# Performance work log

Hardware: AMD Instinct MI355X
Metric: run time of the kernel (lower is better)

## Reference

```python
import jax, jax.numpy as jnp
import numpy as np

F = 26            # number of categorical fields
V_FIELD = 8000    # vocab per field
V = F * V_FIELD   # 208000, size of every shared-index table
D_EMB = 16
DNN_IN = F * F * D_EMB  # 10816
H1, H2 = 256, 128
BS = 4096
NUM_DENSE = 13
EPS = 1e-5


def setup_inputs() -> dict:
    key = jax.random.key(0)
    ks = jax.random.split(key, 16)
    def n(k, shape, s=0.05):
        return jax.random.normal(k, shape, dtype=jnp.float32) * s
    return {
        "X_sparse": jax.random.randint(ks[0], (BS, F), 0, V_FIELD, dtype=jnp.int32),
        "X_dense": jax.random.normal(ks[1], (BS, NUM_DENSE), dtype=jnp.float32),
        "fm1_emb": n(ks[2], (V, 1)),
        "bias": jnp.zeros((1,), jnp.float32),
        "fm1_dense_W": n(ks[3], (1, NUM_DENSE)),
        "fm1_dense_b": jnp.zeros((1,), jnp.float32),
        "emb_tables": n(ks[4], (F, V, D_EMB)),  # one table per field (FFM)
        "dense_W": n(ks[5], (DNN_IN, NUM_DENSE)),
        "dense_b": jnp.zeros((DNN_IN,), jnp.float32),
        "W1": n(ks[6], (H1, DNN_IN)),
        "b1": jnp.zeros((H1,), jnp.float32),
        "g1": jnp.ones((H1,), jnp.float32),
        "beta1": jnp.zeros((H1,), jnp.float32),
        "W2": n(ks[7], (H2, H1)),
        "b2": jnp.zeros((H2,), jnp.float32),
        "g2": jnp.ones((H2,), jnp.float32),
        "beta2": jnp.zeros((H2,), jnp.float32),
        "Wout": n(ks[8], (1, H2)),
        "bout": jnp.zeros((1,), jnp.float32),
    }


def _bn(x, g, b):
    # BatchNorm1d in training mode: biased batch statistics
    m = jnp.mean(x, axis=0)
    v = jnp.var(x, axis=0)
    return (x - m) * jax.lax.rsqrt(v + EPS) * g + b


def reference(X_sparse, X_dense, fm1_emb, bias, fm1_dense_W, fm1_dense_b,
              emb_tables, dense_W, dense_b,
              W1, b1, g1, beta1, W2, b2, g2, beta2, Wout, bout):
    offsets = (jnp.arange(F, dtype=X_sparse.dtype) * V_FIELD)[None, :]
    X = X_sparse + offsets                      # [bs, F] global indices

    # FM first order
    fm1 = jnp.sum(fm1_emb[X], axis=1) + bias    # [bs, 1]
    fm1 = fm1 + X_dense @ fm1_dense_W.T + fm1_dense_b

    # FFM second order: E[t, b, f, d] = table t looked up at field f's index
    E = emb_tables[:, X, :]                     # [F, bs, F, d]
    A = jnp.transpose(E, (1, 0, 2, 3))          # [bs, F_table, F_field, d]
    # pair (i<j): xs[j][:, i] * xs[i][:, j] = A[b, i, j] * A[b, j, i]
    P = A * jnp.swapaxes(A, 1, 2)               # [bs, F, F, d]
    mask = jnp.triu(jnp.ones((F, F), jnp.float32), 1)
    fm2 = jnp.einsum('bijd,ij->b', P, mask)[:, None]  # [bs, 1]

    # DNN: concat per-table lookups then flatten -> [bs, F*F*d]
    dnn = A.reshape(A.shape[0], DNN_IN)
    dnn = dnn + jax.nn.relu(X_dense @ dense_W.T + dense_b)
    h = jax.nn.relu(_bn(dnn @ W1.T + b1, g1, beta1))  # dropout is identity (eval)
    h = jax.nn.relu(_bn(h @ W2.T + b2, g2, beta2))
    out = h @ Wout.T + bout
    return jax.nn.sigmoid(fm1 + fm2 + out)
```

## Files before the change

### kernel.cpp

```cpp
#include <hip/hip_runtime.h>

typedef __bf16 bf16x8 __attribute__((ext_vector_type(8)));
typedef float f32x4 __attribute__((ext_vector_type(4)));

#define F_FIELDS 26
#define V_FIELD  8000
#define V_TOT    208000
#define D_EMBD   16
#define DNN_IN   10816
#define BS       4096
#define ND       13
#define H1_DIM   256
#define H2_DIM   128
#define NP1      8

__device__ __forceinline__ unsigned short f2bf(float f) {
  unsigned u = __float_as_uint(f);
  u += 0x7fffu + ((u >> 16) & 1u);
  return (unsigned short)(u >> 16);
}
__device__ __forceinline__ float bf2f(unsigned short h) {
  return __uint_as_float(((unsigned)h) << 16);
}
__device__ __forceinline__ float bflo(unsigned u) { return __uint_as_float(u << 16); }
__device__ __forceinline__ float bfhi(unsigned u) { return __uint_as_float(u & 0xffff0000u); }
__device__ __forceinline__ unsigned packbf(float a, float b) {
  return (unsigned)f2bf(a) | ((unsigned)f2bf(b) << 16);
}

__device__ __forceinline__ void gload16(const void* g, void* l) {
  __builtin_amdgcn_global_load_lds(
      (const __attribute__((address_space(1))) unsigned int*)g,
      (__attribute__((address_space(3))) unsigned int*)l, 16, 0, 0);
}

__device__ __forceinline__ float dot8bf(uint4 a, uint4 b) {
  const unsigned* pa = (const unsigned*)&a;
  const unsigned* pb = (const unsigned*)&b;
  float s = 0.f;
#pragma unroll
  for (int k = 0; k < 4; ++k)
    s += bflo(pa[k]) * bflo(pb[k]) + bfhi(pa[k]) * bfhi(pb[k]);
  return s;
}

__global__ __launch_bounds__(256) void k_gather(
    const int* __restrict__ Xs, const float* __restrict__ emb,
    const float* __restrict__ fm1_emb, const float* __restrict__ bias,
    const float* __restrict__ fm1dW, const float* __restrict__ fm1db,
    const float* __restrict__ Xd,
    const float* __restrict__ W1, const float* __restrict__ W2,
    unsigned short* __restrict__ W1b, unsigned short* __restrict__ W2b,
    unsigned short* __restrict__ Abf, float* __restrict__ fm12) {
  const int b = blockIdx.x;
  const int tid = threadIdx.x;
  const int lane = tid & 63, wave = tid >> 6;
  __shared__ int   sidx[F_FIELDS];
  __shared__ float sc1[F_FIELDS];
  __shared__ __align__(16) unsigned short As[676 * 16];
  __shared__ float wred[4];

  if (tid < F_FIELDS) {
    int v = Xs[b * F_FIELDS + tid] + tid * V_FIELD;
    sidx[tid] = v;
    sc1[tid] = fm1_emb[v];
  }
  __syncthreads();

  const int q = tid & 3, rbase = tid >> 2;
  float4 vv[11];
#pragma unroll
  for (int it = 0; it < 11; ++it) {
    int r = rbase + it * 64;
    if (r < 676) {
      int i = r / 26, j = r - i * 26;
      const float* src = emb + ((size_t)i * V_TOT + sidx[j]) * D_EMBD + q * 4;
      vv[it] = *(const float4*)src;
    }
  }
  const int n1 = H1_DIM * DNN_IN, n2 = H2_DIM * H1_DIM;
  for (int t = b * 256 + tid; t < n1 + n2; t += BS * 256) {
    if (t < n1) W1b[t] = f2bf(W1[t]);
    else        W2b[t - n1] = f2bf(W2[t - n1]);
  }
#pragma unroll
  for (int it = 0; it < 11; ++it) {
    int r = rbase + it * 64;
    if (r < 676) {
      ushort4 u;
      u.x = f2bf(vv[it].x); u.y = f2bf(vv[it].y);
      u.z = f2bf(vv[it].z); u.w = f2bf(vv[it].w);
      *(ushort4*)&As[r * 16 + q * 4] = u;
      *(ushort4*)&Abf[(size_t)b * DNN_IN + r * 16 + q * 4] = u;
    }
  }
  __syncthreads();

  float acc2 = 0.f;
  for (int p = tid; p < 325; p += 256) {
    float disc = sqrtf((float)(2601 - 8 * p));
    int i = (int)((51.f - disc) * 0.5f);
    int cum = 25 * i - ((i * (i - 1)) >> 1);
    int j = i + 1 + (p - cum);
    const unsigned short* r1 = &As[(i * 26 + j) * 16];
    const unsigned short* r2 = &As[(j * 26 + i) * 16];
    acc2 += dot8bf(*(const uint4*)r1, *(const uint4*)r2);
    acc2 += dot8bf(*(const uint4*)(r1 + 8), *(const uint4*)(r2 + 8));
  }
#pragma unroll
  for (int off = 32; off; off >>= 1) acc2 += __shfl_down(acc2, off);
  if (lane == 0) wred[wave] = acc2;
  __syncthreads();
  if (tid == 0) {
    float fm2 = wred[0] + wred[1] + wred[2] + wred[3];
    float f1 = bias[0] + fm1db[0];
#pragma unroll
    for (int j = 0; j < F_FIELDS; ++j) f1 += sc1[j];
    for (int k = 0; k < ND; ++k) f1 += Xd[b * ND + k] * fm1dW[k];
    fm12[b] = f1 + fm2;
  }
}

__global__ __launch_bounds__(256) void k_dense(
    const float* __restrict__ Xd, const float* __restrict__ dW,
    const float* __restrict__ db_, unsigned short* __restrict__ Dnn) {
  const int t = threadIdx.x;
  const int eg = blockIdx.x * 256 + t;
  const int y0 = blockIdx.y * 64;
  __shared__ float sXd[64 * 13];
  for (int i = t; i < 64 * 13; i += 256) sXd[i] = Xd[y0 * 13 + i];
  __syncthreads();
  if (eg >= DNN_IN / 4) return;
  const int e = eg * 4;
  float wrg[4][13], brg[4];
#pragma unroll
  for (int j = 0; j < 4; ++j) {
    brg[j] = db_[e + j];
#pragma unroll
    for (int k = 0; k < 13; ++k) wrg[j][k] = dW[(e + j) * 13 + k];
  }
  uint2* dp = (uint2*)Dnn;
  for (int s0 = 0; s0 < 64; s0 += 8) {
    uint2 v[8];
#pragma unroll
    for (int u = 0; u < 8; ++u)
      v[u] = dp[(size_t)(y0 + s0 + u) * (DNN_IN / 4) + eg];
#pragma unroll
    for (int u = 0; u < 8; ++u) {
      const float* xr = &sXd[(s0 + u) * 13];
      float d0 = brg[0], d1 = brg[1], d2 = brg[2], d3 = brg[3];
#pragma unroll
      for (int k = 0; k < 13; ++k) {
        float xk = xr[k];
        d0 += wrg[0][k] * xk; d1 += wrg[1][k] * xk;
        d2 += wrg[2][k] * xk; d3 += wrg[3][k] * xk;
      }
      float a0 = bflo(v[u].x) + fmaxf(d0, 0.f);
      float a1 = bfhi(v[u].x) + fmaxf(d1, 0.f);
      float a2 = bflo(v[u].y) + fmaxf(d2, 0.f);
      float a3 = bfhi(v[u].y) + fmaxf(d3, 0.f);
      uint2 o; o.x = packbf(a0, a1); o.y = packbf(a2, a3);
      dp[(size_t)(y0 + s0 + u) * (DNN_IN / 4) + eg] = o;
    }
  }
}

__global__ __launch_bounds__(256) void k_gemm1(
    const unsigned short* __restrict__ A, const unsigned short* __restrict__ B,
    float* __restrict__ C) {
  __shared__ __align__(16) unsigned short sA[3][64 * 32];
  __shared__ __align__(16) unsigned short sB[3][256 * 32];
  const int tid = threadIdx.x;
  const int lane = tid & 63, w = tid >> 6;
  const int id = blockIdx.x;
  const int p = id & 7, mt = id >> 3;
  const int m0 = mt * 64;
  const int s0 = (338 * p) >> 3, s1 = (338 * (p + 1)) >> 3;
  C += (size_t)p * ((size_t)BS * H1_DIM);

  const int q = tid & 3, rr = tid >> 2;
  const unsigned short* gA  = A + (size_t)(m0 + rr) * DNN_IN + q * 8;
  const unsigned short* gB0 = B + (size_t)rr * DNN_IN + q * 8;
  const int fr = lane & 15, fk = lane >> 4;
  const int oA = fr * 32 + fk * 8;
  const int oB = (w * 64 + fr) * 32 + fk * 8;

  f32x4 acc[4][4] = {};

#define STAGE1(ks, bi) do { const int ko_ = (ks) * 32;                      \
    gload16(gA + ko_, &sA[bi][tid * 8]);                                    \
    gload16(gB0 + ko_, &sB[bi][tid * 8]);                                   \
    gload16(gB0 + (size_t)64 * DNN_IN + ko_, &sB[bi][2048 + tid * 8]);      \
    gload16(gB0 + (size_t)128 * DNN_IN + ko_, &sB[bi][4096 + tid * 8]);     \
    gload16(gB0 + (size_t)192 * DNN_IN + ko_, &sB[bi][6144 + tid * 8]); } while (0)

  STAGE1(s0, 0);
  if (s0 + 1 < s1) STAGE1(s0 + 1, 1);
  if (s0 + 2 < s1) STAGE1(s0 + 2, 2);

  int bi = 0;
  for (int ks = s0; ks < s1; ++ks) {
    if (ks + 2 < s1)      asm volatile("s_waitcnt vmcnt(10)" ::: "memory");
    else if (ks + 1 < s1) asm volatile("s_waitcnt vmcnt(5)" ::: "memory");
    else                  asm volatile("s_waitcnt vmcnt(0)" ::: "memory");
    __builtin_amdgcn_sched_barrier(0);
    __builtin_amdgcn_s_barrier();
    bf16x8 av[4], bv[4];
#pragma unroll
    for (int mi = 0; mi < 4; ++mi) av[mi] = *(const bf16x8*)&sA[bi][oA + mi * 512];
#pragma unroll
    for (int ni = 0; ni < 4; ++ni) bv[ni] = *(const bf16x8*)&sB[bi][oB + ni * 512];
    asm volatile("s_waitcnt lgkmcnt(0)" ::: "memory");
    __builtin_amdgcn_sched_barrier(0);
    __builtin_amdgcn_s_barrier();
    if (ks + 3 < s1) STAGE1(ks + 3, bi);
#pragma unroll
    for (int mi = 0; mi < 4; ++mi)
#pragma unroll
      for (int ni = 0; ni < 4; ++ni)
        acc[mi][ni] = __builtin_amdgcn_mfma_f32_16x16x32_bf16(
            av[mi], bv[ni], acc[mi][ni], 0, 0, 0);
    bi = bi + 1; if (bi == 3) bi = 0;
  }
#pragma unroll
  for (int mi = 0; mi < 4; ++mi)
#pragma unroll
    for (int ni = 0; ni < 4; ++ni)
#pragma unroll
      for (int r = 0; r < 4; ++r) {
        int row = m0 + mi * 16 + fk * 4 + r;
        int col = w * 64 + ni * 16 + fr;
        C[(size_t)row * H1_DIM + col] = acc[mi][ni][r];
      }
#undef STAGE1
}

__global__ __launch_bounds__(256) void k_stat1(
    const float* __restrict__ Yp, const float* __restrict__ b1,
    float* __restrict__ Y1, float* __restrict__ ps, float* __restrict__ pq) {
  const int g = blockIdx.x, n = threadIdx.x;
  const size_t plane = (size_t)BS * H1_DIM;
  float s = 0.f, s2 = 0.f;
  float bn = b1[n];
  for (int bb = 0; bb < 16; ++bb) {
    size_t o = (size_t)(g * 16 + bb) * H1_DIM + n;
    float y = bn;
#pragma unroll
    for (int pp = 0; pp < NP1; ++pp) y += Yp[o + pp * plane];
    Y1[o] = y; s += y; s2 += y * y;
  }
  ps[g * H1_DIM + n] = s;
  pq[g * H1_DIM + n] = s2;
}

__global__ __launch_bounds__(256) void k_apply1(
    const float* __restrict__ Y1, const float* __restrict__ ps,
    const float* __restrict__ pq, const float* __restrict__ g1,
    const float* __restrict__ be1, unsigned short* __restrict__ H1b) {
  const int g = blockIdx.x, n = threadIdx.x;
  float s = 0.f, s2 = 0.f;
  for (int gg = 0; gg < 256; ++gg) {
    s += ps[gg * H1_DIM + n];
    s2 += pq[gg * H1_DIM + n];
  }
  float m = s * (1.f / BS);
  float v = s2 * (1.f / BS) - m * m;
  float r = rsqrtf(v + 1e-5f);
  float ga = g1[n], bb_ = be1[n];
  for (int bb = 0; bb < 16; ++bb) {
    size_t o = (size_t)(g * 16 + bb) * H1_DIM + n;
    float h = (Y1[o] - m) * r * ga + bb_;
    H1b[o] = f2bf(fmaxf(h, 0.f));
  }
}

__global__ __launch_bounds__(256) void k_gemm2(
    const unsigned short* __restrict__ A, const unsigned short* __restrict__ B,
    const float* __restrict__ b2, float* __restrict__ Y2,
    float* __restrict__ ps, float* __restrict__ pq) {
  __shared__ __align__(16) unsigned short sA[2][128 * 32];
  __shared__ __align__(16) unsigned short sB[2][128 * 32];
  __shared__ float redS[8][H2_DIM];
  __shared__ float redQ[8][H2_DIM];
  const int tid = threadIdx.x;
  const int lane = tid & 63, wave = tid >> 6;
  const int m0 = blockIdx.x * 128;

  const int q = tid & 3, rr = tid >> 2;
  const unsigned short* gA0 = A + (size_t)(m0 + rr) * H1_DIM + q * 8;
  const unsigned short* gA1 = gA0 + (size_t)64 * H1_DIM;
  const unsigned short* gB0 = B + (size_t)rr * H1_DIM + q * 8;
  const unsigned short* gB1 = gB0 + (size_t)64 * H1_DIM;
  const int lo = wave * 512;

  const int wr = wave >> 1, wc = wave & 1;
  const int fr = lane & 15, fk = lane >> 4;
  const int oA = (wr * 64 + fr) * 32 + fk * 8;
  const int oB = (wc * 64 + fr) * 32 + fk * 8;

  f32x4 acc[4][4] = {};
  {
    gload16(gA0, &sA[0][lo]);
    gload16(gA1, &sA[0][2048 + lo]);
    gload16(gB0, &sB[0][lo]);
    gload16(gB1, &sB[0][2048 + lo]);
  }
  for (int ks = 0; ks < 8; ++ks) {
    const int cur = ks & 1;
    if (ks + 1 < 8) {
      const int ko = (ks + 1) * 32;
      gload16(gA0 + ko, &sA[cur ^ 1][lo]);
      gload16(gA1 + ko, &sA[cur ^ 1][2048 + lo]);
      gload16(gB0 + ko, &sB[cur ^ 1][lo]);
      gload16(gB1 + ko, &sB[cur ^ 1][2048 + lo]);
      asm volatile("s_waitcnt vmcnt(4)" ::: "memory");
    } else {
      asm volatile("s_waitcnt vmcnt(0)" ::: "memory");
    }
    __builtin_amdgcn_sched_barrier(0);
    __builtin_amdgcn_s_barrier();
    bf16x8 av[4], bv[4];
#pragma unroll
    for (int mi = 0; mi < 4; ++mi) av[mi] = *(const bf16x8*)&sA[cur][oA + mi * 512];
#pragma unroll
    for (int ni = 0; ni < 4; ++ni) bv[ni] = *(const bf16x8*)&sB[cur][oB + ni * 512];
    asm volatile("s_waitcnt lgkmcnt(0)" ::: "memory");
    __builtin_amdgcn_sched_barrier(0);
    __builtin_amdgcn_s_barrier();
#pragma unroll
    for (int mi = 0; mi < 4; ++mi)
#pragma unroll
      for (int ni = 0; ni < 4; ++ni)
        acc[mi][ni] = __builtin_amdgcn_mfma_f32_16x16x32_bf16(
            av[mi], bv[ni], acc[mi][ni], 0, 0, 0);
  }
  float sc[4] = {0.f, 0.f, 0.f, 0.f}, sq[4] = {0.f, 0.f, 0.f, 0.f};
#pragma unroll
  for (int ni = 0; ni < 4; ++ni) {
    int col = wc * 64 + ni * 16 + fr;
    float bcol = b2[col];
#pragma unroll
    for (int mi = 0; mi < 4; ++mi)
#pragma unroll
      for (int r = 0; r < 4; ++r) {
        int row = m0 + wr * 64 + mi * 16 + fk * 4 + r;
        float y = acc[mi][ni][r] + bcol;
        Y2[(size_t)row * H2_DIM + col] = y;
        sc[ni] += y; sq[ni] += y * y;
      }
  }
  const int slot = wr * 4 + fk;
#pragma unroll
  for (int ni = 0; ni < 4; ++ni) {
    int col = wc * 64 + ni * 16 + fr;
    redS[slot][col] = sc[ni];
    redQ[slot][col] = sq[ni];
  }
  __syncthreads();
  if (tid < H2_DIM) {
    float s = 0.f, s2 = 0.f;
#pragma unroll
    for (int sl = 0; sl < 8; ++sl) { s += redS[sl][tid]; s2 += redQ[sl][tid]; }
    ps[blockIdx.x * H2_DIM + tid] = s;
    pq[blockIdx.x * H2_DIM + tid] = s2;
  }
}

__global__ __launch_bounds__(256) void k_final(
    const float* __restrict__ Y2, const float* __restrict__ ps,
    const float* __restrict__ pq, const float* __restrict__ g2,
    const float* __restrict__ be2, const float* __restrict__ Wout,
    const float* __restrict__ bout, const float* __restrict__ fm12,
    float* __restrict__ out) {
  const int tid = threadIdx.x, wave = tid >> 6, lane = tid & 63;
  __shared__ float sm[H2_DIM], sr[H2_DIM], sg[H2_DIM], sbe[H2_DIM], sw[H2_DIM];
  if (tid < H2_DIM) {
    float s = 0.f, s2 = 0.f;
    for (int g = 0; g < 32; ++g) {
      s += ps[g * H2_DIM + tid];
      s2 += pq[g * H2_DIM + tid];
    }
    float m = s * (1.f / BS);
    float v = s2 * (1.f / BS) - m * m;
    sm[tid] = m; sr[tid] = rsqrtf(v + 1e-5f);
    sg[tid] = g2[tid]; sbe[tid] = be2[tid]; sw[tid] = Wout[tid];
  }
  __syncthreads();
  const float bo = bout[0];
  for (int ii = 0; ii < 16; ++ii) {
    int s = blockIdx.x * 64 + wave * 16 + ii;
    float acc = 0.f;
#pragma unroll
    for (int nn = 0; nn < 2; ++nn) {
      int n = lane + nn * 64;
      float y = Y2[(size_t)s * H2_DIM + n];
      float h = (y - sm[n]) * sr[n] * sg[n] + sbe[n];
      acc += fmaxf(h, 0.f) * sw[n];
    }
#pragma unroll
    for (int off = 32; off; off >>= 1) acc += __shfl_down(acc, off);
    if (lane == 0) {
      float logit = fm12[s] + acc + bo;
      out[s] = 1.f / (1.f + expf(-logit));
    }
  }
}

extern "C" void kernel_launch(void* const* d_in, const int* in_sizes, int n_in,
                              void* d_out, int out_size, void* d_ws, size_t ws_size,
                              hipStream_t stream) {
  const int*   Xs     = (const int*)d_in[0];
  const float* Xd     = (const float*)d_in[1];
  const float* fm1e   = (const float*)d_in[2];
  const float* bias   = (const float*)d_in[3];
  const float* fm1dW  = (const float*)d_in[4];
  const float* fm1db  = (const float*)d_in[5];
  const float* emb    = (const float*)d_in[6];
  const float* dW     = (const float*)d_in[7];
  const float* db_    = (const float*)d_in[8];
  const float* W1     = (const float*)d_in[9];
  const float* b1     = (const float*)d_in[10];
  const float* g1     = (const float*)d_in[11];
  const float* be1    = (const float*)d_in[12];
  const float* W2     = (const float*)d_in[13];
  const float* b2     = (const float*)d_in[14];
  const float* g2     = (const float*)d_in[15];
  const float* be2    = (const float*)d_in[16];
  const float* Wout   = (const float*)d_in[17];
  const float* bout   = (const float*)d_in[18];
  float* out = (float*)d_out;

  char* w = (char*)d_ws;
  unsigned short* Dnn = (unsigned short*)w; w += (size_t)BS * DNN_IN * 2;
  unsigned short* W1b = (unsigned short*)w; w += (size_t)H1_DIM * DNN_IN * 2;
  unsigned short* W2b = (unsigned short*)w; w += (size_t)H2_DIM * H1_DIM * 2;
  float* fm12 = (float*)w;  w += (size_t)BS * 4;
  float* Ypart = (float*)w; w += (size_t)NP1 * BS * H1_DIM * 4;
  float* Y1 = (float*)w;    w += (size_t)BS * H1_DIM * 4;
  unsigned short* H1b = (unsigned short*)w; w += (size_t)BS * H1_DIM * 2;
  float* Y2 = (float*)w;    w += (size_t)BS * H2_DIM * 4;
  float* ps1 = (float*)w;   w += 256 * H1_DIM * 4;
  float* pq1 = (float*)w;   w += 256 * H1_DIM * 4;
  float* ps2 = (float*)w;   w += 32 * H2_DIM * 4;
  float* pq2 = (float*)w;   w += 32 * H2_DIM * 4;

  k_gather<<<BS, 256, 0, stream>>>(Xs, emb, fm1e, bias, fm1dW, fm1db, Xd,
                                   W1, W2, W1b, W2b, Dnn, fm12);
  k_dense<<<dim3(11, 64), 256, 0, stream>>>(Xd, dW, db_, Dnn);
  k_gemm1<<<64 * NP1, 256, 0, stream>>>(Dnn, W1b, Ypart);
  k_stat1<<<256, 256, 0, stream>>>(Ypart, b1, Y1, ps1, pq1);
  k_apply1<<<256, 256, 0, stream>>>(Y1, ps1, pq1, g1, be1, H1b);
  k_gemm2<<<32, 256, 0, stream>>>(H1b, W2b, b2, Y2, ps2, pq2);
  k_final<<<BS / 64, 256, 0, stream>>>(Y2, ps2, pq2, g2, be2, Wout, bout, fm12, out);
}
```

Measured before the change: 213.0 us.

## Fuse dense-feature projection into GEMM1 via per-tile MFMA recompute

Removes the separate k_dense kernel, which read and rewrote the whole bf16 activation matrix. GEMM1 now computes relu(Xd·dW^T+db) on the fly for each K-tile with small MFMAs, using Xd padded with a bias column of ones and a bf16 dW laid out K-major. It then accumulates that tile against W1 as a second MFMA pass. This saves a full read-modify-write pass over the large activation buffer, at the cost of extra MFMAs, an extra LDS round trip and barrier per K step, and extra global loads in the pipeline.

```diff
diff --git a/kernel.cpp b/kernel.cpp
--- a/kernel.cpp
+++ b/kernel.cpp
@@ -24,9 +24,6 @@
 }
 __device__ __forceinline__ float bflo(unsigned u) { return __uint_as_float(u << 16); }
 __device__ __forceinline__ float bfhi(unsigned u) { return __uint_as_float(u & 0xffff0000u); }
-__device__ __forceinline__ unsigned packbf(float a, float b) {
-  return (unsigned)f2bf(a) | ((unsigned)f2bf(b) << 16);
-}
 
 __device__ __forceinline__ void gload16(const void* g, void* l) {
   __builtin_amdgcn_global_load_lds(
@@ -50,7 +47,9 @@
     const float* __restrict__ fm1dW, const float* __restrict__ fm1db,
     const float* __restrict__ Xd,
     const float* __restrict__ W1, const float* __restrict__ W2,
+    const float* __restrict__ dW, const float* __restrict__ db_,
     unsigned short* __restrict__ W1b, unsigned short* __restrict__ W2b,
+    unsigned short* __restrict__ dWb,
     unsigned short* __restrict__ Abf, float* __restrict__ fm12) {
   const int b = blockIdx.x;
   const int tid = threadIdx.x;
@@ -82,6 +81,16 @@
   for (int t = b * 256 + tid; t < n1 + n2; t += BS * 256) {
     if (t < n1) W1b[t] = f2bf(W1[t]);
     else        W2b[t - n1] = f2bf(W2[t - n1]);
+  }
+  for (int e = b * 256 + tid; e < DNN_IN; e += BS * 256) {
+    unsigned short row[32];
+#pragma unroll
+    for (int k = 0; k < 13; ++k) row[k] = f2bf(dW[e * 13 + k]);
+    row[13] = f2bf(db_[e]);
+#pragma unroll
+    for (int k = 14; k < 32; ++k) row[k] = 0;
+#pragma unroll
+    for (int k = 0; k < 32; ++k) dWb[e * 32 + k] = row[k];
   }
 #pragma unroll
   for (int it = 0; it < 11; ++it) {
@@ -121,55 +130,15 @@
   }
 }
 
-__global__ __launch_bounds__(256) void k_dense(
-    const float* __restrict__ Xd, const float* __restrict__ dW,
-    const float* __restrict__ db_, unsigned short* __restrict__ Dnn) {
-  const int t = threadIdx.x;
-  const int eg = blockIdx.x * 256 + t;
-  const int y0 = blockIdx.y * 64;
-  __shared__ float sXd[64 * 13];
-  for (int i = t; i < 64 * 13; i += 256) sXd[i] = Xd[y0 * 13 + i];
-  __syncthreads();
-  if (eg >= DNN_IN / 4) return;
-  const int e = eg * 4;
-  float wrg[4][13], brg[4];
-#pragma unroll
-  for (int j = 0; j < 4; ++j) {
-    brg[j] = db_[e + j];
-#pragma unroll
-    for (int k = 0; k < 13; ++k) wrg[j][k] = dW[(e + j) * 13 + k];
-  }
-  uint2* dp = (uint2*)Dnn;
-  for (int s0 = 0; s0 < 64; s0 += 8) {
-    uint2 v[8];
-#pragma unroll
-    for (int u = 0; u < 8; ++u)
-      v[u] = dp[(size_t)(y0 + s0 + u) * (DNN_IN / 4) + eg];
-#pragma unroll
-    for (int u = 0; u < 8; ++u) {
-      const float* xr = &sXd[(s0 + u) * 13];
-      float d0 = brg[0], d1 = brg[1], d2 = brg[2], d3 = brg[3];
-#pragma unroll
-      for (int k = 0; k < 13; ++k) {
-        float xk = xr[k];
-        d0 += wrg[0][k] * xk; d1 += wrg[1][k] * xk;
-        d2 += wrg[2][k] * xk; d3 += wrg[3][k] * xk;
-      }
-      float a0 = bflo(v[u].x) + fmaxf(d0, 0.f);
-      float a1 = bfhi(v[u].x) + fmaxf(d1, 0.f);
-      float a2 = bflo(v[u].y) + fmaxf(d2, 0.f);
-      float a3 = bfhi(v[u].y) + fmaxf(d3, 0.f);
-      uint2 o; o.x = packbf(a0, a1); o.y = packbf(a2, a3);
-      dp[(size_t)(y0 + s0 + u) * (DNN_IN / 4) + eg] = o;
-    }
-  }
-}
-
 __global__ __launch_bounds__(256) void k_gemm1(
     const unsigned short* __restrict__ A, const unsigned short* __restrict__ B,
+    const unsigned short* __restrict__ dWb, const float* __restrict__ Xd,
     float* __restrict__ C) {
   __shared__ __align__(16) unsigned short sA[3][64 * 32];
   __shared__ __align__(16) unsigned short sB[3][256 * 32];
+  __shared__ __align__(16) unsigned short sWd[3][1024];
+  __shared__ __align__(16) unsigned short sD[64 * 32];
+  __shared__ __align__(16) unsigned short sXd[64 * 32];
   const int tid = threadIdx.x;
   const int lane = tid & 63, w = tid >> 6;
   const int id = blockIdx.x;
@@ -178,6 +147,19 @@
   const int s0 = (338 * p) >> 3, s1 = (338 * (p + 1)) >> 3;
   C += (size_t)p * ((size_t)BS * H1_DIM);
 
+  if (tid < 64) {
+    const float* xr = Xd + (size_t)(m0 + tid) * ND;
+    unsigned short row[32];
+#pragma unroll
+    for (int k = 0; k < 13; ++k) row[k] = f2bf(xr[k]);
+    row[13] = 0x3F80;
+#pragma unroll
+    for (int k = 14; k < 32; ++k) row[k] = 0;
+#pragma unroll
+    for (int k = 0; k < 32; ++k) sXd[tid * 32 + k] = row[k];
+  }
+  __syncthreads();
+
   const int q = tid & 3, rr = tid >> 2;
   const unsigned short* gA  = A + (size_t)(m0 + rr) * DNN_IN + q * 8;
   const unsigned short* gB0 = B + (size_t)rr * DNN_IN + q * 8;
@@ -185,14 +167,23 @@
   const int oA = fr * 32 + fk * 8;
   const int oB = (w * 64 + fr) * 32 + fk * 8;
 
+  const bf16x8 avd = *(const bf16x8*)&sXd[(w * 16 + fr) * 32 + fk * 8];
+  const int oW0 = fr * 32 + fk * 8;
+  const int oW1 = (16 + fr) * 32 + fk * 8;
+  const int drow = w * 16 + fk * 4;
+
   f32x4 acc[4][4] = {};
+  const f32x4 zf = {0.f, 0.f, 0.f, 0.f};
 
 #define STAGE1(ks, bi) do { const int ko_ = (ks) * 32;                      \
     gload16(gA + ko_, &sA[bi][tid * 8]);                                    \
     gload16(gB0 + ko_, &sB[bi][tid * 8]);                                   \
     gload16(gB0 + (size_t)64 * DNN_IN + ko_, &sB[bi][2048 + tid * 8]);      \
     gload16(gB0 + (size_t)128 * DNN_IN + ko_, &sB[bi][4096 + tid * 8]);     \
-    gload16(gB0 + (size_t)192 * DNN_IN + ko_, &sB[bi][6144 + tid * 8]); } while (0)
+    gload16(gB0 + (size_t)192 * DNN_IN + ko_, &sB[bi][6144 + tid * 8]);     \
+    gload16(dWb + (size_t)ko_ * 32 + (size_t)lane * 8, &sWd[bi][lane * 8]); \
+    gload16(dWb + (size_t)ko_ * 32 + 512 + (size_t)lane * 8,                \
+            &sWd[bi][512 + lane * 8]); } while (0)
 
   STAGE1(s0, 0);
   if (s0 + 1 < s1) STAGE1(s0 + 1, 1);
@@ -200,11 +191,13 @@
 
   int bi = 0;
   for (int ks = s0; ks < s1; ++ks) {
-    if (ks + 2 < s1)      asm volatile("s_waitcnt vmcnt(10)" ::: "memory");
-    else if (ks + 1 < s1) asm volatile("s_waitcnt vmcnt(5)" ::: "memory");
+    if (ks + 2 < s1)      asm volatile("s_waitcnt vmcnt(14)" ::: "memory");
+    else if (ks + 1 < s1) asm volatile("s_waitcnt vmcnt(7)" ::: "memory");
     else                  asm volatile("s_waitcnt vmcnt(0)" ::: "memory");
     __builtin_amdgcn_sched_barrier(0);
     __builtin_amdgcn_s_barrier();
+    bf16x8 bw0 = *(const bf16x8*)&sWd[bi][oW0];
+    bf16x8 bw1 = *(const bf16x8*)&sWd[bi][oW1];
     bf16x8 av[4], bv[4];
 #pragma unroll
     for (int mi = 0; mi < 4; ++mi) av[mi] = *(const bf16x8*)&sA[bi][oA + mi * 512];
@@ -212,14 +205,34 @@
     for (int ni = 0; ni < 4; ++ni) bv[ni] = *(const bf16x8*)&sB[bi][oB + ni * 512];
     asm volatile("s_waitcnt lgkmcnt(0)" ::: "memory");
     __builtin_amdgcn_sched_barrier(0);
-    __builtin_amdgcn_s_barrier();
-    if (ks + 3 < s1) STAGE1(ks + 3, bi);
+    f32x4 d0 = __builtin_amdgcn_mfma_f32_16x16x32_bf16(avd, bw0, zf, 0, 0, 0);
+    f32x4 d1 = __builtin_amdgcn_mfma_f32_16x16x32_bf16(avd, bw1, zf, 0, 0, 0);
 #pragma unroll
     for (int mi = 0; mi < 4; ++mi)
 #pragma unroll
       for (int ni = 0; ni < 4; ++ni)
         acc[mi][ni] = __builtin_amdgcn_mfma_f32_16x16x32_bf16(
             av[mi], bv[ni], acc[mi][ni], 0, 0, 0);
+#pragma unroll
+    for (int r = 0; r < 4; ++r) {
+      sD[(drow + r) * 32 + fr]      = f2bf(fmaxf(d0[r], 0.f));
+      sD[(drow + r) * 32 + 16 + fr] = f2bf(fmaxf(d1[r], 0.f));
+    }
+    asm volatile("s_waitcnt lgkmcnt(0)" ::: "memory");
+    __builtin_amdgcn_sched_barrier(0);
+    __builtin_amdgcn_s_barrier();
+    if (ks + 3 < s1) STAGE1(ks + 3, bi);
+    bf16x8 dv[4];
+#pragma unroll
+    for (int mi = 0; mi < 4; ++mi) dv[mi] = *(const bf16x8*)&sD[oA + mi * 512];
+    asm volatile("s_waitcnt lgkmcnt(0)" ::: "memory");
+    __builtin_amdgcn_sched_barrier(0);
+#pragma unroll
+    for (int mi = 0; mi < 4; ++mi)
+#pragma unroll
+      for (int ni = 0; ni < 4; ++ni)
+        acc[mi][ni] = __builtin_amdgcn_mfma_f32_16x16x32_bf16(
+            dv[mi], bv[ni], acc[mi][ni], 0, 0, 0);
     bi = bi + 1; if (bi == 3) bi = 0;
   }
 #pragma unroll
@@ -434,6 +447,7 @@
   unsigned short* Dnn = (unsigned short*)w; w += (size_t)BS * DNN_IN * 2;
   unsigned short* W1b = (unsigned short*)w; w += (size_t)H1_DIM * DNN_IN * 2;
   unsigned short* W2b = (unsigned short*)w; w += (size_t)H2_DIM * H1_DIM * 2;
+  unsigned short* dWb = (unsigned short*)w; w += (size_t)DNN_IN * 32 * 2;
   float* fm12 = (float*)w;  w += (size_t)BS * 4;
   float* Ypart = (float*)w; w += (size_t)NP1 * BS * H1_DIM * 4;
   float* Y1 = (float*)w;    w += (size_t)BS * H1_DIM * 4;
@@ -445,9 +459,8 @@
   float* pq2 = (float*)w;   w += 32 * H2_DIM * 4;
 
   k_gather<<<BS, 256, 0, stream>>>(Xs, emb, fm1e, bias, fm1dW, fm1db, Xd,
-                                   W1, W2, W1b, W2b, Dnn, fm12);
-  k_dense<<<dim3(11, 64), 256, 0, stream>>>(Xd, dW, db_, Dnn);
-  k_gemm1<<<64 * NP1, 256, 0, stream>>>(Dnn, W1b, Ypart);
+                                   W1, W2, dW, db_, W1b, W2b, dWb, Dnn, fm12);
+  k_gemm1<<<64 * NP1, 256, 0, stream>>>(Dnn, W1b, dWb, Xd, Ypart);
   k_stat1<<<256, 256, 0, stream>>>(Ypart, b1, Y1, ps1, pq1);
   k_apply1<<<256, 256, 0, stream>>>(Y1, ps1, pq1, g1, be1, H1b);
   k_gemm2<<<32, 256, 0, stream>>>(H1b, W2b, b2, Y2, ps2, pq2);
```

Result: faster. 187.1 us (-12.2%).
